# Optimization experiments

Measured on AMD Instinct MI355X. Metric: run time of the kernel, lower is better.

Reference implementation:

```python
import jax, jax.numpy as jnp
import numpy as np

D_IN, H, NH = 256, 512, 8
B, T = 8, 1024


def sinusoidal_pe(seq_len, d_model):
    pos = jnp.arange(seq_len, dtype=jnp.float32)[:, None]
    div = jnp.exp(jnp.arange(0, d_model, 2, dtype=jnp.float32) * (-jnp.log(10000.0) / d_model))
    pe = jnp.zeros((seq_len, d_model), jnp.float32)
    pe = pe.at[:, 0::2].set(jnp.sin(pos * div)).at[:, 1::2].set(jnp.cos(pos * div))
    return pe


def layer_norm(x, g, b, eps=1e-5):
    mu = jnp.mean(x, -1, keepdims=True)
    var = jnp.mean((x - mu) ** 2, -1, keepdims=True)
    return (x - mu) * jax.lax.rsqrt(var + eps) * g + b


def lstm_dir(x, wih, whh, bih, bhh):
    # x: [B,T,H]; wih/whh: [4H,H]; gate order i,f,g,o (PyTorch convention)
    Bx = x.shape[0]
    Hh = whh.shape[1]
    xg = jnp.einsum('bth,gh->btg', x, wih) + bih  # precompute input gates [B,T,4H]

    def step(carry, xg_t):
        h, c = carry
        gates = xg_t + h @ whh.T + bhh
        i, f, g, o = jnp.split(gates, 4, axis=-1)
        c = jax.nn.sigmoid(f) * c + jax.nn.sigmoid(i) * jnp.tanh(g)
        h = jax.nn.sigmoid(o) * jnp.tanh(c)
        return (h, c), h

    h0 = jnp.zeros((Bx, Hh), x.dtype)
    _, hs = jax.lax.scan(step, (h0, h0), xg.transpose(1, 0, 2))
    return hs.transpose(1, 0, 2)  # [B,T,H]


def setup_inputs():
    key = jax.random.key(0)
    ks = jax.random.split(key, 30)
    s = 0.02

    def g(k, shape):
        return jax.random.normal(k, shape, jnp.float32) * s

    return {
        'temporal_data': jax.random.normal(ks[0], (B, T, D_IN), jnp.float32),
        'w_in': g(ks[1], (H, D_IN)), 'b_in': jnp.zeros((H,), jnp.float32),
        'wq': g(ks[2], (H, H)), 'bq': jnp.zeros((H,), jnp.float32),
        'wk': g(ks[3], (H, H)), 'bk': jnp.zeros((H,), jnp.float32),
        'wv': g(ks[4], (H, H)), 'bv': jnp.zeros((H,), jnp.float32),
        'wo': g(ks[5], (H, H)), 'bo': jnp.zeros((H,), jnp.float32),
        'g1': jnp.ones((H,), jnp.float32), 'b1': jnp.zeros((H,), jnp.float32),
        'wih_f': g(ks[6], (4 * H, H)), 'whh_f': g(ks[7], (4 * H, H)),
        'bih_f': jnp.zeros((4 * H,), jnp.float32), 'bhh_f': jnp.zeros((4 * H,), jnp.float32),
        'wih_b': g(ks[8], (4 * H, H)), 'whh_b': g(ks[9], (4 * H, H)),
        'bih_b': jnp.zeros((4 * H,), jnp.float32), 'bhh_b': jnp.zeros((4 * H,), jnp.float32),
        'g2': jnp.ones((2 * H,), jnp.float32), 'b2': jnp.zeros((2 * H,), jnp.float32),
        'w_out': g(ks[10], (H, 2 * H)), 'b_out': jnp.zeros((H,), jnp.float32),
    }


def reference(temporal_data, w_in, b_in, wq, bq, wk, bk, wv, bv, wo, bo, g1, b1,
              wih_f, whh_f, bih_f, bhh_f, wih_b, whh_b, bih_b, bhh_b, g2, b2, w_out, b_out):
    x = temporal_data @ w_in.T + b_in                      # [B,T,H]
    Bx, Tx, _ = x.shape
    x = x + sinusoidal_pe(Tx, H)
    residual = x

    hd = H // NH
    q = (x @ wq.T + bq).reshape(Bx, Tx, NH, hd).transpose(0, 2, 1, 3)
    k = (x @ wk.T + bk).reshape(Bx, Tx, NH, hd).transpose(0, 2, 1, 3)
    v = (x @ wv.T + bv).reshape(Bx, Tx, NH, hd).transpose(0, 2, 1, 3)
    scores = jnp.einsum('bhqd,bhkd->bhqk', q, k) * (hd ** -0.5)
    causal = jnp.triu(jnp.ones((Tx, Tx), bool), 1)
    scores = jnp.where(causal, jnp.float32(-1e9), scores)
    attn = jax.nn.softmax(scores, axis=-1)
    o = jnp.einsum('bhqk,bhkd->bhqd', attn, v).transpose(0, 2, 1, 3).reshape(Bx, Tx, H)
    o = o @ wo.T + bo

    x = layer_norm(o + residual, g1, b1)                   # dropout in eval = identity

    h_fwd = lstm_dir(x, wih_f, whh_f, bih_f, bhh_f)
    h_bwd = jnp.flip(lstm_dir(jnp.flip(x, 1), wih_b, whh_b, bih_b, bhh_b), 1)
    lstm_out = jnp.concatenate([h_fwd, h_bwd], axis=-1)    # [B,T,2H]
    lstm_out = layer_norm(lstm_out, g2, b2)

    emb = jnp.mean(lstm_out, axis=1)                       # [B,2H]
    return emb @ w_out.T + b_out                           # [B,H]
```

## Files before the change

### kernel.cpp

```cpp
#include <hip/hip_runtime.h>

typedef unsigned short u16;
typedef unsigned int   u32;
typedef unsigned long long u64;
typedef __attribute__((ext_vector_type(8))) short short8v;
typedef __attribute__((ext_vector_type(4))) float f32x4;
typedef __attribute__((ext_vector_type(4))) unsigned int u32x4;

#define DINL __device__ __forceinline__

DINL u16 f2bf(float f){ union{float f;u32 u;} v{f}; return (u16)((v.u + 0x7fffu + ((v.u>>16)&1u))>>16); }
DINL float bf2f(u16 b){ union{u32 u;float f;} v{(u32)b<<16}; return v.f; }
DINL f32x4 MFMA16(short8v a, short8v b, f32x4 c){ return __builtin_amdgcn_mfma_f32_16x16x32_bf16(a,b,c,0,0,0); }
DINL void gl16(const void* g, void* l){
  __builtin_amdgcn_global_load_lds((const __attribute__((address_space(1))) void*)g,
                                   (__attribute__((address_space(3))) void*)l, 16, 0, 0);
}
DINL float wredd(float v){
#pragma unroll
  for (int m=1;m<64;m<<=1) v += __shfl_xor(v, m);
  return v;
}
DINL float sigm(float x){ return 1.f/(1.f+__expf(-x)); }
DINL float tanh_(float x){ return 2.f/(1.f+__expf(-2.f*x)) - 1.f; }

__global__ __launch_bounds__(256) void zerok(u32* __restrict__ dst){
  size_t i = ((size_t)blockIdx.x*256 + threadIdx.x)*4;
  u32x4 z = {0,0,0,0};
  *(u32x4*)(dst + i) = z;
}

__global__ __launch_bounds__(256) void cvtk(const float* __restrict__ src, u16* __restrict__ dst, int n){
  int i = (blockIdx.x*256 + threadIdx.x)*4;
  float4 v = *(const float4*)(src + i);
  dst[i+0]=f2bf(v.x); dst[i+1]=f2bf(v.y); dst[i+2]=f2bf(v.z); dst[i+3]=f2bf(v.w);
}

template<int EPI>
__global__ __launch_bounds__(256) void gemm128(
    const u16* __restrict__ A, const u16* __restrict__ W,
    const float* __restrict__ bias0, const float* __restrict__ bias1, const float* __restrict__ bias2,
    const u16* __restrict__ resid, u16* __restrict__ out, int M, int N, int K)
{
  __shared__ __align__(16) u16 Al[128*64];
  __shared__ __align__(16) u16 Bl[128*64];
  const int tid = threadIdx.x, lane = tid & 63, w = tid >> 6;
  const int wr = w >> 1, wc = w & 1;
  const int m0 = blockIdx.y * 128, n0 = blockIdx.x * 128;
  f32x4 acc[4][4] = {};
  for (int k0 = 0; k0 < K; k0 += 64) {
#pragma unroll
    for (int j = 0; j < 4; ++j) {
      int idx = (j*4 + w)*64 + lane;
      int r = idx >> 3, c8 = idx & 7;
      gl16(A + (size_t)(m0 + r)*K + k0 + c8*8, (void*)(Al + (size_t)(j*4+w)*512));
      gl16(W + (size_t)(n0 + r)*K + k0 + c8*8, (void*)(Bl + (size_t)(j*4+w)*512));
    }
    __syncthreads();
#pragma unroll
    for (int kk = 0; kk < 2; ++kk) {
      short8v af[4], bf[4];
#pragma unroll
      for (int i = 0; i < 4; ++i)
        af[i] = *(const short8v*)(Al + ((wr*64 + i*16 + (lane&15))*64 + kk*32 + (lane>>4)*8));
#pragma unroll
      for (int i = 0; i < 4; ++i)
        bf[i] = *(const short8v*)(Bl + ((wc*64 + i*16 + (lane&15))*64 + kk*32 + (lane>>4)*8));
#pragma unroll
      for (int mi=0;mi<4;++mi)
#pragma unroll
        for (int ni=0;ni<4;++ni)
          acc[mi][ni] = MFMA16(af[mi], bf[ni], acc[mi][ni]);
    }
    __syncthreads();
  }
#pragma unroll
  for (int mi=0;mi<4;++mi)
#pragma unroll
    for (int ni=0;ni<4;++ni)
#pragma unroll
      for (int r=0;r<4;++r) {
        int m = m0 + wr*64 + mi*16 + (lane>>4)*4 + r;
        int n = n0 + wc*64 + ni*16 + (lane&15);
        float v = acc[mi][ni][r];
        if constexpr (EPI == 0) {
          int t = m & 1023;
          float ang = (float)t * expf((float)(n & ~1) * (-9.210340371976184f/512.f));
          v += bias0[n] + ((n & 1) ? cosf(ang) : sinf(ang));
          out[(size_t)m*512 + n] = f2bf(v);
        } else if constexpr (EPI == 1) {
          int g = n >> 9, n5 = n & 511, hh = n5 >> 6, dh = n5 & 63;
          v += (g==0 ? bias0 : g==1 ? bias1 : bias2)[n5];
          size_t bh = (size_t)((m>>10)*8 + hh);
          u16 val = f2bf(v);
          if (g == 0)      out[(bh*1024 + (m&1023))*64 + dh] = val;
          else if (g == 1) out[4194304 + (bh*1024 + (m&1023))*64 + dh] = val;
          else             out[8388608 + (bh*64 + dh)*1024 + (m&1023)] = val;
        } else {
          v += bias0[n] + bf2f(resid[(size_t)m*512 + n]);
          out[(size_t)m*512 + n] = f2bf(v);
        }
      }
}

__global__ __launch_bounds__(256) void attnk(const u16* __restrict__ qb, const u16* __restrict__ kb,
                                             const u16* __restrict__ vt, u16* __restrict__ attno)
{
  __shared__ __align__(16) u16 P[4][16][72];
  const int tid = threadIdx.x, lane = tid & 63, w = tid >> 6;
  const int bh = blockIdx.x >> 4, qblk = blockIdx.x & 15;
  const int b = bh >> 3, h = bh & 7;
  const float scale = 0.125f;
  short8v qf[2];
  {
    const u16* qbase = qb + ((size_t)bh*1024 + qblk*64 + w*16)*64;
#pragma unroll
    for (int kk=0;kk<2;++kk)
      qf[kk] = *(const short8v*)(qbase + (size_t)(lane&15)*64 + kk*32 + (lane>>4)*8);
  }
  f32x4 o[4] = {};
  float mrun[4], lrun[4];
#pragma unroll
  for (int r=0;r<4;++r){ mrun[r] = -1e30f; lrun[r] = 0.f; }
  for (int kblk = 0; kblk <= qblk; ++kblk) {
    f32x4 s[4] = {};
#pragma unroll
    for (int kk=0;kk<2;++kk)
#pragma unroll
      for (int nt=0;nt<4;++nt) {
        short8v kf = *(const short8v*)(kb + ((size_t)bh*1024 + kblk*64 + nt*16 + (lane&15))*64 + kk*32 + (lane>>4)*8);
        s[nt] = MFMA16(qf[kk], kf, s[nt]);
      }
    float pnew[4][4];
#pragma unroll
    for (int r=0;r<4;++r) {
      int q = qblk*64 + w*16 + (lane>>4)*4 + r;
      float sv[4]; float rowmax = -1e30f;
#pragma unroll
      for (int nt=0;nt<4;++nt) {
        int key = kblk*64 + nt*16 + (lane&15);
        float x = s[nt][r]*scale;
        if (key > q) x = -1e30f;
        sv[nt] = x; rowmax = fmaxf(rowmax, x);
      }
#pragma unroll
      for (int msk=1; msk<16; msk<<=1) rowmax = fmaxf(rowmax, __shfl_xor(rowmax, msk));
      float mnew = fmaxf(mrun[r], rowmax);
      float sf = __expf(mrun[r]-mnew);
      float psum = 0.f;
#pragma unroll
      for (int nt=0;nt<4;++nt){ float p = __expf(sv[nt]-mnew); pnew[nt][r]=p; psum += p; }
#pragma unroll
      for (int msk=1; msk<16; msk<<=1) psum += __shfl_xor(psum, msk);
      lrun[r] = lrun[r]*sf + psum;
      mrun[r] = mnew;
#pragma unroll
      for (int nt=0;nt<4;++nt) o[nt][r] *= sf;
    }
#pragma unroll
    for (int nt=0;nt<4;++nt)
#pragma unroll
      for (int r=0;r<4;++r)
        P[w][(lane>>4)*4+r][nt*16+(lane&15)] = f2bf(pnew[nt][r]);
#pragma unroll
    for (int kk=0;kk<2;++kk) {
      short8v pf = *(const short8v*)&P[w][lane&15][kk*32 + (lane>>4)*8];
#pragma unroll
      for (int nt=0;nt<4;++nt) {
        short8v vf = *(const short8v*)(vt + ((size_t)bh*64 + nt*16 + (lane&15))*1024 + kblk*64 + kk*32 + (lane>>4)*8);
        o[nt] = MFMA16(pf, vf, o[nt]);
      }
    }
  }
#pragma unroll
  for (int nt=0;nt<4;++nt)
#pragma unroll
    for (int r=0;r<4;++r) {
      int q = qblk*64 + w*16 + (lane>>4)*4 + r;
      int dh = nt*16 + (lane&15);
      attno[((size_t)b*1024 + q)*512 + h*64 + dh] = f2bf(o[nt][r] / lrun[r]);
    }
}

__global__ __launch_bounds__(256) void ln1k(const u16* __restrict__ pre, const float* __restrict__ g1,
                                            const float* __restrict__ b1, u16* __restrict__ xl){
  int row = blockIdx.x*4 + (threadIdx.x>>6), lane = threadIdx.x&63;
  short8v xv = *(const short8v*)(pre + (size_t)row*512 + lane*8);
  float v[8], s=0.f, s2=0.f;
#pragma unroll
  for (int e=0;e<8;++e){ v[e]=bf2f((u16)xv[e]); s+=v[e]; s2+=v[e]*v[e]; }
  s = wredd(s); s2 = wredd(s2);
  float mu = s*(1.f/512.f);
  float rs = rsqrtf(s2*(1.f/512.f) - mu*mu + 1e-5f);
  int b = row>>10, t = row&1023;
  short8v ov;
#pragma unroll
  for (int e=0;e<8;++e){ int c=lane*8+e; ov[e]=(short)f2bf((v[e]-mu)*rs*g1[c]+b1[c]); }
  *(short8v*)(xl + ((size_t)t*8 + b)*512 + lane*8) = ov;
}

__global__ __launch_bounds__(512) void lstmk(
    const u16* __restrict__ xl,
    const float* __restrict__ wih_f, const float* __restrict__ whh_f,
    const float* __restrict__ bih_f, const float* __restrict__ bhh_f,
    const float* __restrict__ wih_b, const float* __restrict__ whh_b,
    const float* __restrict__ bih_b, const float* __restrict__ bhh_b,
    u32* __restrict__ hx, u16* __restrict__ hs)
{
  extern __shared__ float RED[];

  const int tid = threadIdx.x, lane = tid&63, w = tid>>6;
  const int d = blockIdx.x >> 4, slice = blockIdx.x & 15, u0 = slice*32;
  const float* WIHg = d ? wih_b : wih_f;
  const float* WHHg = d ? whh_b : whh_f;
  const float* BIH  = d ? bih_b : bih_f;
  const float* BHH  = d ? bhh_b : bhh_f;

  const int l15 = lane&15, l16 = lane>>4;

  short8v wi[8][2], wh[8][2];
#pragma unroll
  for (int nt=0; nt<8; ++nt) {
    const int g = nt>>1, uh = nt&1;
    const size_t row = (size_t)(g*512 + u0 + uh*16 + l15);
#pragma unroll
    for (int kk=0; kk<2; ++kk) {
      const int k = w*64 + kk*32 + l16*8;
      const float* pi = WIHg + row*512 + k;
      const float* ph = WHHg + row*512 + k;
      float4 a0 = *(const float4*)pi, a1 = *(const float4*)(pi+4);
      float4 b0 = *(const float4*)ph, b1 = *(const float4*)(ph+4);
      short8v si, sh;
      si[0]=(short)f2bf(a0.x); si[1]=(short)f2bf(a0.y); si[2]=(short)f2bf(a0.z); si[3]=(short)f2bf(a0.w);
      si[4]=(short)f2bf(a1.x); si[5]=(short)f2bf(a1.y); si[6]=(short)f2bf(a1.z); si[7]=(short)f2bf(a1.w);
      sh[0]=(short)f2bf(b0.x); sh[1]=(short)f2bf(b0.y); sh[2]=(short)f2bf(b0.z); sh[3]=(short)f2bf(b0.w);
      sh[4]=(short)f2bf(b1.x); sh[5]=(short)f2bf(b1.y); sh[6]=(short)f2bf(b1.z); sh[7]=(short)f2bf(b1.w);
      wi[nt][kk] = si; wh[nt][kk] = sh;
    }
  }

  const bool act = tid < 256;
  const int b_ = tid>>5, u_ = tid&31;
  float c_state = 0.f, bias_c[4];
  if (act)
#pragma unroll
    for (int g=0;g<4;++g) bias_c[g] = BIH[g*512+u0+u_] + BHH[g*512+u0+u_];

  __syncthreads();

  for (int t = 0; t < 1024; ++t) {
    const int te = d ? 1023 - t : t;
    f32x4 acc[8] = {};
    {
      const u16* xb = xl + ((size_t)te*8 + (lane&7))*512 + w*64 + l16*8;
      short8v xf0 = *(const short8v*)(xb);
      short8v xf1 = *(const short8v*)(xb + 32);
#pragma unroll
      for (int nt=0; nt<8; ++nt) acc[nt] = MFMA16(xf0, wi[nt][0], acc[nt]);
#pragma unroll
      for (int nt=0; nt<8; ++nt) acc[nt] = MFMA16(xf1, wi[nt][1], acc[nt]);
    }
    if (t > 0) {
      const u32 tg = (u32)t;
      const u32* pb = hx + ((size_t)d*2 + ((t-1)&1))*4096 + (size_t)(lane&7)*512 + w*64 + l16*8;
      u32x4 q0,q1,q2,q3;
      for (;;) {
        asm volatile(
          "global_load_dwordx4 %0, %4, off sc0 sc1\n\t"
          "global_load_dwordx4 %1, %4, off offset:16 sc0 sc1\n\t"
          "global_load_dwordx4 %2, %4, off offset:128 sc0 sc1\n\t"
          "global_load_dwordx4 %3, %4, off offset:144 sc0 sc1\n\t"
          "s_waitcnt vmcnt(0)"
          : "=&v"(q0),"=&v"(q1),"=&v"(q2),"=&v"(q3)
          : "v"(pb));
        bool ok = true;
#pragma unroll
        for (int e=0;e<4;++e) {
          ok = ok && ((q0[e]&0xffffu)==tg) && ((q1[e]&0xffffu)==tg)
                  && ((q2[e]&0xffffu)==tg) && ((q3[e]&0xffffu)==tg);
        }
        if (__all(ok)) break;
        __builtin_amdgcn_s_sleep(1);
      }
      short8v hf0, hf1;
#pragma unroll
      for (int e=0;e<4;++e) {
        hf0[e]   = (short)(q0[e] >> 16);
        hf0[4+e] = (short)(q1[e] >> 16);
        hf1[e]   = (short)(q2[e] >> 16);
        hf1[4+e] = (short)(q3[e] >> 16);
      }
#pragma unroll
      for (int nt=0; nt<8; ++nt) acc[nt] = MFMA16(hf0, wh[nt][0], acc[nt]);
#pragma unroll
      for (int nt=0; nt<8; ++nt) acc[nt] = MFMA16(hf1, wh[nt][1], acc[nt]);
    }
    float* R = RED + (size_t)(t & 1)*9216;
    if (lane < 32)
#pragma unroll
      for (int nt=0; nt<8; ++nt)
#pragma unroll
        for (int rg=0; rg<4; ++rg)
          R[(((size_t)nt*4 + rg)*32 + lane)*9 + w] = acc[nt][rg];
    __syncthreads();
    if (act) {
      const int uh = u_>>4, lc = (u_&15) + 16*(b_>>2), rg = b_&3;
      float gates[4];
#pragma unroll
      for (int g=0;g<4;++g) {
        const float* q = R + (((size_t)(g*2+uh)*4 + rg)*32 + lc)*9;
        gates[g] = ((q[0]+q[1])+(q[2]+q[3])) + ((q[4]+q[5])+(q[6]+q[7])) + bias_c[g];
      }
      float ig = sigm(gates[0]), fg = sigm(gates[1]), gg = tanh_(gates[2]), og = sigm(gates[3]);
      c_state = fg*c_state + ig*gg;
      u16 hv = f2bf(og * tanh_(c_state));
      u32 word = ((u32)hv << 16) | (u32)(t + 1);
      u32* dst = hx + ((size_t)d*2 + (t&1))*4096 + (size_t)b_*512 + u0 + u_;
      (void)__hip_atomic_exchange(dst, word, __ATOMIC_RELAXED, __HIP_MEMORY_SCOPE_AGENT);
      hs[((size_t)(d*1024 + te)*8 + b_)*512 + u0 + u_] = hv;
    }
  }
}

__global__ __launch_bounds__(256) void ln2k(const u16* __restrict__ hs, const float* __restrict__ g2,
                                            const float* __restrict__ b2, float* __restrict__ emb){
  __shared__ float accl[4][1024];
  int b = blockIdx.x>>4, chunk = blockIdx.x&15;
  int lane = threadIdx.x&63, w = threadIdx.x>>6;
  for (int i=lane;i<1024;i+=64) accl[w][i]=0.f;
#pragma unroll 1
  for (int i=0;i<16;++i) {
    int t = chunk*64 + w*16 + i;
    short8v xf = *(const short8v*)(hs + ((size_t)t*8 + b)*512 + lane*8);
    short8v xb = *(const short8v*)(hs + ((size_t)(1024+t)*8 + b)*512 + lane*8);
    float vf[8], vb[8], s=0.f, s2=0.f;
#pragma unroll
    for (int e=0;e<8;++e){ vf[e]=bf2f((u16)xf[e]); vb[e]=bf2f((u16)xb[e]);
                           s += vf[e]+vb[e]; s2 += vf[e]*vf[e]+vb[e]*vb[e]; }
    s = wredd(s); s2 = wredd(s2);
    float mu = s*(1.f/1024.f);
    float rs = rsqrtf(s2*(1.f/1024.f) - mu*mu + 1e-5f);
#pragma unroll
    for (int e=0;e<8;++e){
      int c = lane*8+e;
      accl[w][c]     += (vf[e]-mu)*rs*g2[c]     + b2[c];
      accl[w][512+c] += (vb[e]-mu)*rs*g2[512+c] + b2[512+c];
    }
  }
  __syncthreads();
  for (int c = threadIdx.x; c < 1024; c += 256)
    atomicAdd(emb + (size_t)b*1024 + c, accl[0][c]+accl[1][c]+accl[2][c]+accl[3][c]);
}

__global__ __launch_bounds__(256) void fink(const float* __restrict__ emb, const float* __restrict__ w_out,
                                            const float* __restrict__ b_out, float* __restrict__ out){
  int gid = blockIdx.x*256 + threadIdx.x;
  int n = gid>>3, b = gid&7;
  const float* e = emb + (size_t)b*1024;
  const float* wr = w_out + (size_t)n*1024;
  float s = 0.f;
  for (int k=0;k<1024;k+=4) {
    float4 ev = *(const float4*)(e+k);
    float4 wv = *(const float4*)(wr+k);
    s += ev.x*wv.x + ev.y*wv.y + ev.z*wv.z + ev.w*wv.w;
  }
  out[(size_t)b*512 + n] = b_out[n] + s*(1.f/1024.f);
}

#define OFF_EMB   0u
#define OFF_HX    32768u
#define OFF_A0    98304u
#define OFF_WIN   4292608u
#define OFF_WQKV  4554752u
#define OFF_WO    6127616u
#define OFF_X0B   6651904u
#define OFF_QB    15040512u
#define OFF_PRE   15040512u
#define OFF_XL    23429120u
#define OFF_ATT   40206336u
#define OFF_HS    48594944u

extern "C" void kernel_launch(void* const* d_in, const int* in_sizes, int n_in,
                              void* d_out, int out_size, void* d_ws, size_t ws_size,
                              hipStream_t stream) {
  const float* temporal = (const float*)d_in[0];
  const float* w_in = (const float*)d_in[1];  const float* b_in = (const float*)d_in[2];
  const float* wq = (const float*)d_in[3];    const float* bq = (const float*)d_in[4];
  const float* wk = (const float*)d_in[5];    const float* bk = (const float*)d_in[6];
  const float* wv = (const float*)d_in[7];    const float* bv = (const float*)d_in[8];
  const float* wo = (const float*)d_in[9];    const float* bo = (const float*)d_in[10];
  const float* g1 = (const float*)d_in[11];   const float* b1 = (const float*)d_in[12];
  const float* wih_f = (const float*)d_in[13]; const float* whh_f = (const float*)d_in[14];
  const float* bih_f = (const float*)d_in[15]; const float* bhh_f = (const float*)d_in[16];
  const float* wih_b = (const float*)d_in[17]; const float* whh_b = (const float*)d_in[18];
  const float* bih_b = (const float*)d_in[19]; const float* bhh_b = (const float*)d_in[20];
  const float* g2 = (const float*)d_in[21];   const float* b2 = (const float*)d_in[22];
  const float* w_out = (const float*)d_in[23]; const float* b_out = (const float*)d_in[24];

  char* ws = (char*)d_ws;
  float* EMB = (float*)(ws + OFF_EMB);
  u32* HX   = (u32*)(ws + OFF_HX);
  u16* A0   = (u16*)(ws + OFF_A0);
  u16* WIN  = (u16*)(ws + OFF_WIN);
  u16* WQKV = (u16*)(ws + OFF_WQKV);
  u16* WOb  = (u16*)(ws + OFF_WO);
  u16* X0B  = (u16*)(ws + OFF_X0B);
  u16* QB   = (u16*)(ws + OFF_QB);
  u16* PRE  = (u16*)(ws + OFF_PRE);
  u16* XL   = (u16*)(ws + OFF_XL);
  u16* ATT  = (u16*)(ws + OFF_ATT);
  u16* HS   = (u16*)(ws + OFF_HS);

  (void)hipFuncSetAttribute((const void*)lstmk, hipFuncAttributeMaxDynamicSharedMemorySize, 73728);

  zerok<<<24,256,0,stream>>>((u32*)(ws + OFF_EMB));

  cvtk<<<2048,256,0,stream>>>(temporal, A0, 2097152);
  cvtk<<<128, 256,0,stream>>>(w_in, WIN, 131072);
  cvtk<<<256, 256,0,stream>>>(wq, WQKV,           262144);
  cvtk<<<256, 256,0,stream>>>(wk, WQKV + 262144,  262144);
  cvtk<<<256, 256,0,stream>>>(wv, WQKV + 524288,  262144);
  cvtk<<<256, 256,0,stream>>>(wo, WOb, 262144);

  gemm128<0><<<dim3(4,64), 256, 0, stream>>>(A0, WIN, b_in, nullptr, nullptr, nullptr, X0B, 8192, 512, 256);
  gemm128<1><<<dim3(12,64),256, 0, stream>>>(X0B, WQKV, bq, bk, bv, nullptr, QB, 8192, 1536, 512);
  attnk<<<1024,256,0,stream>>>(QB, QB + 4194304, QB + 8388608, ATT);
  gemm128<3><<<dim3(4,64), 256, 0, stream>>>(ATT, WOb, bo, nullptr, nullptr, X0B, PRE, 8192, 512, 512);
  ln1k<<<2048,256,0,stream>>>(PRE, g1, b1, XL);
  lstmk<<<32,512,73728,stream>>>(XL, wih_f, whh_f, bih_f, bhh_f, wih_b, whh_b, bih_b, bhh_b, HX, HS);
  ln2k<<<128,256,0,stream>>>(HS, g2, b2, EMB);
  fink<<<16,256,0,stream>>>(EMB, w_out, b_out, (float*)d_out);
}
```

Baseline: 4.221 ms.

## Replace tagged-word polling with per-slice flags and packed bf16 hidden state

```diff
diff --git a/kernel.cpp b/kernel.cpp
--- a/kernel.cpp
+++ b/kernel.cpp
@@ -6,6 +6,7 @@
 typedef __attribute__((ext_vector_type(8))) short short8v;
 typedef __attribute__((ext_vector_type(4))) float f32x4;
 typedef __attribute__((ext_vector_type(4))) unsigned int u32x4;
+typedef __attribute__((ext_vector_type(2))) unsigned int u32x2;
 
 #define DINL __device__ __forceinline__
 
@@ -205,7 +206,7 @@
     const float* __restrict__ bih_f, const float* __restrict__ bhh_f,
     const float* __restrict__ wih_b, const float* __restrict__ whh_b,
     const float* __restrict__ bih_b, const float* __restrict__ bhh_b,
-    u32* __restrict__ hx, u16* __restrict__ hs)
+    u16* __restrict__ hx2, u32* __restrict__ flg, u16* __restrict__ hs)
 {
   extern __shared__ float RED[];
 
@@ -250,6 +251,11 @@
 
   for (int t = 0; t < 1024; ++t) {
     const int te = d ? 1023 - t : t;
+    const u32 tg = (u32)t;
+    const u32* fb = flg + ((size_t)d*2 + ((t-1)&1))*16 + 2*w;
+    u32x2 fpair;
+    if (t > 0)
+      asm volatile("global_load_dwordx2 %0, %1, off sc0 sc1" : "=&v"(fpair) : "v"(fb));
     f32x4 acc[8] = {};
     {
       const u16* xb = xl + ((size_t)te*8 + (lane&7))*512 + w*64 + l16*8;
@@ -261,35 +267,21 @@
       for (int nt=0; nt<8; ++nt) acc[nt] = MFMA16(xf1, wi[nt][1], acc[nt]);
     }
     if (t > 0) {
-      const u32 tg = (u32)t;
-      const u32* pb = hx + ((size_t)d*2 + ((t-1)&1))*4096 + (size_t)(lane&7)*512 + w*64 + l16*8;
-      u32x4 q0,q1,q2,q3;
-      for (;;) {
-        asm volatile(
-          "global_load_dwordx4 %0, %4, off sc0 sc1\n\t"
-          "global_load_dwordx4 %1, %4, off offset:16 sc0 sc1\n\t"
-          "global_load_dwordx4 %2, %4, off offset:128 sc0 sc1\n\t"
-          "global_load_dwordx4 %3, %4, off offset:144 sc0 sc1\n\t"
-          "s_waitcnt vmcnt(0)"
-          : "=&v"(q0),"=&v"(q1),"=&v"(q2),"=&v"(q3)
-          : "v"(pb));
-        bool ok = true;
-#pragma unroll
-        for (int e=0;e<4;++e) {
-          ok = ok && ((q0[e]&0xffffu)==tg) && ((q1[e]&0xffffu)==tg)
-                  && ((q2[e]&0xffffu)==tg) && ((q3[e]&0xffffu)==tg);
-        }
-        if (__all(ok)) break;
+      asm volatile("s_waitcnt vmcnt(0)" : "+v"(fpair));
+      while (!__all(fpair[0]==tg && fpair[1]==tg)) {
         __builtin_amdgcn_s_sleep(1);
-      }
-      short8v hf0, hf1;
-#pragma unroll
-      for (int e=0;e<4;++e) {
-        hf0[e]   = (short)(q0[e] >> 16);
-        hf0[4+e] = (short)(q1[e] >> 16);
-        hf1[e]   = (short)(q2[e] >> 16);
-        hf1[4+e] = (short)(q3[e] >> 16);
-      }
+        asm volatile("global_load_dwordx2 %0, %1, off sc0 sc1\n\ts_waitcnt vmcnt(0)"
+                     : "=&v"(fpair) : "v"(fb));
+      }
+      const u16* pb2 = hx2 + ((size_t)d*2 + ((t-1)&1))*4096 + (size_t)(lane&7)*512 + w*64 + l16*8;
+      u32x4 r0, r1;
+      asm volatile(
+        "global_load_dwordx4 %0, %2, off sc0 sc1\n\t"
+        "global_load_dwordx4 %1, %2, off offset:64 sc0 sc1\n\t"
+        "s_waitcnt vmcnt(0)"
+        : "=&v"(r0), "=&v"(r1) : "v"(pb2));
+      short8v hf0 = __builtin_bit_cast(short8v, r0);
+      short8v hf1 = __builtin_bit_cast(short8v, r1);
 #pragma unroll
       for (int nt=0; nt<8; ++nt) acc[nt] = MFMA16(hf0, wh[nt][0], acc[nt]);
 #pragma unroll
@@ -314,10 +306,15 @@
       float ig = sigm(gates[0]), fg = sigm(gates[1]), gg = tanh_(gates[2]), og = sigm(gates[3]);
       c_state = fg*c_state + ig*gg;
       u16 hv = f2bf(og * tanh_(c_state));
-      u32 word = ((u32)hv << 16) | (u32)(t + 1);
-      u32* dst = hx + ((size_t)d*2 + (t&1))*4096 + (size_t)b_*512 + u0 + u_;
-      (void)__hip_atomic_exchange(dst, word, __ATOMIC_RELAXED, __HIP_MEMORY_SCOPE_AGENT);
+      u16* dsth = hx2 + ((size_t)d*2 + (t&1))*4096 + (size_t)b_*512 + u0 + u_;
+      asm volatile("global_store_short %0, %1, off sc0 sc1" :: "v"(dsth), "v"((u32)hv) : "memory");
       hs[((size_t)(d*1024 + te)*8 + b_)*512 + u0 + u_] = hv;
+    }
+    __syncthreads();
+    if (tid == 0) {
+      u32* fdst = flg + ((size_t)d*2 + (t&1))*16 + slice;
+      u32 fv = tg + 1u;
+      asm volatile("global_store_dword %0, %1, off sc0 sc1" :: "v"(fdst), "v"(fv) : "memory");
     }
   }
 }
@@ -368,7 +365,8 @@
 }
 
 #define OFF_EMB   0u
-#define OFF_HX    32768u
+#define OFF_FLG   32768u
+#define OFF_HX2   33024u
 #define OFF_A0    98304u
 #define OFF_WIN   4292608u
 #define OFF_WQKV  4554752u
@@ -399,7 +397,8 @@
 
   char* ws = (char*)d_ws;
   float* EMB = (float*)(ws + OFF_EMB);
-  u32* HX   = (u32*)(ws + OFF_HX);
+  u32* FLG  = (u32*)(ws + OFF_FLG);
+  u16* HX2  = (u16*)(ws + OFF_HX2);
   u16* A0   = (u16*)(ws + OFF_A0);
   u16* WIN  = (u16*)(ws + OFF_WIN);
   u16* WQKV = (u16*)(ws + OFF_WQKV);
@@ -413,7 +412,7 @@
 
   (void)hipFuncSetAttribute((const void*)lstmk, hipFuncAttributeMaxDynamicSharedMemorySize, 73728);
 
-  zerok<<<24,256,0,stream>>>((u32*)(ws + OFF_EMB));
+  zerok<<<9,256,0,stream>>>((u32*)(ws + OFF_EMB));
 
   cvtk<<<2048,256,0,stream>>>(temporal, A0, 2097152);
   cvtk<<<128, 256,0,stream>>>(w_in, WIN, 131072);
@@ -427,7 +426,7 @@
   attnk<<<1024,256,0,stream>>>(QB, QB + 4194304, QB + 8388608, ATT);
   gemm128<3><<<dim3(4,64), 256, 0, stream>>>(ATT, WOb, bo, nullptr, nullptr, X0B, PRE, 8192, 512, 512);
   ln1k<<<2048,256,0,stream>>>(PRE, g1, b1, XL);
-  lstmk<<<32,512,73728,stream>>>(XL, wih_f, whh_f, bih_f, bhh_f, wih_b, whh_b, bih_b, bhh_b, HX, HS);
+  lstmk<<<32,512,73728,stream>>>(XL, wih_f, whh_f, bih_f, bhh_f, wih_b, whh_b, bih_b, bhh_b, HX2, FLG, HS);
   ln2k<<<128,256,0,stream>>>(HS, g2, b2, EMB);
   fink<<<16,256,0,stream>>>(EMB, w_out, b_out, (float*)d_out);
 }
```

Measured after the change: 3.411 ms. -19.2%, faster.
